# Optimization experiments

Measured on AMD Instinct MI355X. Metric: run time of the kernel, lower is better.

Reference implementation:

```python
import jax, jax.numpy as jnp
import numpy as np

N = 200000
E = 600000
C = 256


def setup_inputs() -> dict:
    key = jax.random.key(0)
    k1, k2, k3, k4, k5 = jax.random.split(key, 5)
    x = jax.random.normal(k1, (N, C), dtype=jnp.float32)
    sources = jax.random.randint(k2, (E,), 0, N, dtype=jnp.int64)
    targets = jax.random.randint(k3, (E,), 0, N, dtype=jnp.int64)
    norm = jax.random.uniform(k4, (N, 1), dtype=jnp.float32)
    # xavier_normal for [C, C]: std = sqrt(2 / (fan_in + fan_out))
    std = float(np.sqrt(2.0 / (C + C)))
    weight = jax.random.normal(k5, (C, C), dtype=jnp.float32) * std
    return {"x": x, "sources": sources, "targets": targets, "norm": norm, "weight": weight}


def reference(x, sources, targets, norm, weight):
    # out-of-place index_add: x + scatter_add(x[sources] -> targets)
    agg = x.at[targets].add(x[sources])  # [N, C]
    h = norm * agg                        # [N, C], norm broadcasts over channels
    return h @ weight                     # [N, C]
```

## Files before the change

kernel.cpp:

```cpp
#include <hip/hip_runtime.h>
#include <hip/hip_bf16.h>

#define NN 200000
#define NE 600000
#define CH 256
#define NBLK_SCAN 196

typedef short bf16x8 __attribute__((ext_vector_type(8)));
typedef float f32x4 __attribute__((ext_vector_type(4)));
typedef unsigned short ushort8v __attribute__((ext_vector_type(8)));

__device__ __forceinline__ unsigned short f2bf(float f) {
    unsigned int u = __builtin_bit_cast(unsigned int, f);
    u = (u + 0x7FFFu + ((u >> 16) & 1u)) >> 16;
    return (unsigned short)u;
}
__device__ __forceinline__ float bf2f(unsigned short u) {
    unsigned int v = ((unsigned int)u) << 16;
    return __builtin_bit_cast(float, v);
}

__global__ void k_wt(const float* __restrict__ W, unsigned short* __restrict__ Wt) {
    int j = blockIdx.x, k = threadIdx.x;
    Wt[j * CH + k] = f2bf(W[k * CH + j]);
}

__global__ __launch_bounds__(256) void k_prep(const float* __restrict__ W,
                                              unsigned short* __restrict__ Wt,
                                              const int* __restrict__ te,
                                              int* __restrict__ deg) {
    const int t = blockIdx.x * 256 + threadIdx.x;
    const int S = gridDim.x * 256;
    for (int e = t; e < NE; e += S) atomicAdd(&deg[te[e]], 1);
    for (int i = t; i < CH * CH; i += S) {
        int j = i >> 8, k = i & 255;
        Wt[j * CH + k] = f2bf(W[k * CH + j]);
    }
}

__global__ __launch_bounds__(256) void k_scanA(const int* __restrict__ deg,
                                               int* __restrict__ off,
                                               int* __restrict__ bsum) {
    __shared__ int ts[256];
    int tid = threadIdx.x;
    int base = blockIdx.x * 1024 + tid * 4;
    int v[4];
#pragma unroll
    for (int j = 0; j < 4; ++j) {
        int idx = base + j;
        v[j] = (idx < NN) ? deg[idx] : 0;
    }
    int tsum = v[0] + v[1] + v[2] + v[3];
    ts[tid] = tsum;
    __syncthreads();
    int x = tsum;
    for (int ofs = 1; ofs < 256; ofs <<= 1) {
        int y = (tid >= ofs) ? ts[tid - ofs] : 0;
        __syncthreads();
        x += y;
        ts[tid] = x;
        __syncthreads();
    }
    int run = x - tsum;
#pragma unroll
    for (int j = 0; j < 4; ++j) {
        int idx = base + j;
        if (idx < NN) off[idx] = run;
        run += v[j];
    }
    if (tid == 255) bsum[blockIdx.x] = x;
}

__global__ __launch_bounds__(256) void k_scanC(int* __restrict__ off,
                                               const int* __restrict__ bsum,
                                               int* __restrict__ cur) {
    __shared__ int ts[256];
    int tid = threadIdx.x;
    int v = (tid < NBLK_SCAN) ? bsum[tid] : 0;
    ts[tid] = v;
    __syncthreads();
    int x = v;
    for (int ofs = 1; ofs < 256; ofs <<= 1) {
        int y = (tid >= ofs) ? ts[tid - ofs] : 0;
        __syncthreads();
        x += y;
        ts[tid] = x;
        __syncthreads();
    }
    const int bo = (blockIdx.x == 0) ? 0 : ts[blockIdx.x - 1];
    int base = blockIdx.x * 1024 + tid * 4;
#pragma unroll
    for (int j = 0; j < 4; ++j) {
        int idx = base + j;
        if (idx < NN) {
            int o = off[idx] + bo;
            off[idx] = o;
            cur[idx] = o;
        }
    }
}

__global__ void k_fill(const int* __restrict__ se, const int* __restrict__ te,
                       int* __restrict__ cur, int* __restrict__ elist) {
    int e = blockIdx.x * 256 + threadIdx.x;
    if (e < NE) {
        int t = te[e];
        int pos = atomicAdd(&cur[t], 1);
        elist[pos] = se[e];
    }
}

__global__ __launch_bounds__(512, 4) void k_zw(const float* __restrict__ x,
                                               const unsigned short* __restrict__ Wt,
                                               unsigned short* __restrict__ zbf,
                                               const int* __restrict__ te,
                                               int* __restrict__ deg) {
    __shared__ unsigned short lds_a[128 * CH];
    const int tid = threadIdx.x;
    const int wid = tid >> 6;
    const int lane = tid & 63;
    const int wr = wid >> 2;
    const int wc = wid & 3;
    const int rb = blockIdx.x * 128;
    const int r16 = lane & 15;
    const int q = lane >> 4;
    const int vr = min(128, NN - rb);

    {
        const long long e = (long long)blockIdx.x * 512 + tid;
        if (e < NE) atomicAdd(&deg[te[e]], 1);
    }

#pragma unroll
    for (int i = 0; i < 8; ++i) {
        const int idx = i * 4096 + tid * 8;
        const int row = idx >> 8;
        const int col = idx & 255;
        const int srow = min(rb + row, NN - 1);
        const float* src = x + (size_t)srow * CH + col;
        float4 f0 = *reinterpret_cast<const float4*>(src);
        float4 f1 = *reinterpret_cast<const float4*>(src + 4);
        ushort8v w;
        w[0] = f2bf(f0.x); w[1] = f2bf(f0.y); w[2] = f2bf(f0.z); w[3] = f2bf(f0.w);
        w[4] = f2bf(f1.x); w[5] = f2bf(f1.y); w[6] = f2bf(f1.z); w[7] = f2bf(f1.w);
        const int gs = (col >> 3) ^ (row & 7);
        *reinterpret_cast<ushort8v*>(&lds_a[row * CH + gs * 8]) = w;
    }
    __syncthreads();

    f32x4 acc[4][4];
#pragma unroll
    for (int m = 0; m < 4; ++m)
#pragma unroll
        for (int nt = 0; nt < 4; ++nt) acc[m][nt] = (f32x4){0.f, 0.f, 0.f, 0.f};

    const unsigned short* wb = Wt + (size_t)(wc * 64 + r16) * CH + q * 8;

#pragma unroll
    for (int kk = 0; kk < 8; ++kk) {
        bf16x8 b[4];
#pragma unroll
        for (int nt = 0; nt < 4; ++nt)
            b[nt] = *reinterpret_cast<const bf16x8*>(wb + (size_t)nt * 16 * CH + kk * 32);
        bf16x8 a[4];
#pragma unroll
        for (int m = 0; m < 4; ++m) {
            const int lr = wr * 64 + m * 16 + r16;
            const int aidx = lr * CH + ((((kk * 4) + q) ^ (lr & 7)) << 3);
            a[m] = *reinterpret_cast<const bf16x8*>(&lds_a[aidx]);
        }
#pragma unroll
        for (int m = 0; m < 4; ++m)
#pragma unroll
            for (int nt = 0; nt < 4; ++nt)
                acc[m][nt] = __builtin_amdgcn_mfma_f32_16x16x32_bf16(a[m], b[nt], acc[m][nt], 0, 0, 0);
    }

    __syncthreads();
#pragma unroll
    for (int m = 0; m < 4; ++m) {
#pragma unroll
        for (int nt = 0; nt < 4; ++nt) {
            const int zr = wr * 64 + m * 16 + q * 4;
            const int zc = wc * 64 + nt * 16 + r16;
#pragma unroll
            for (int r = 0; r < 4; ++r)
                lds_a[(zr + r) * CH + zc] = f2bf(acc[m][nt][r]);
        }
    }
    __syncthreads();
    unsigned short* zdst = zbf + (size_t)rb * CH;
#pragma unroll
    for (int j = 0; j < 8; ++j) {
        const int idx = j * 4096 + tid * 8;
        const int row = idx >> 8;
        if (row < vr)
            *reinterpret_cast<ushort8v*>(zdst + idx) =
                *reinterpret_cast<const ushort8v*>(&lds_a[idx]);
    }
}

__global__ __launch_bounds__(256) void k_gout(const unsigned short* __restrict__ zbf,
                                              const int* __restrict__ off,
                                              const int* __restrict__ deg,
                                              const int* __restrict__ elist,
                                              const float* __restrict__ norm,
                                              float* __restrict__ out) {
    int wid = threadIdx.x >> 6;
    int lane = threadIdx.x & 63;
    int row = blockIdx.x * 4 + wid;
    if (row >= NN) return;
    int start = off[row];
    int d = deg[row];
    const int uo = lane * 4;
    ushort4 bv = *reinterpret_cast<const ushort4*>(zbf + (size_t)row * CH + uo);
    float ax = bf2f(bv.x), ay = bf2f(bv.y), az = bf2f(bv.z), aw = bf2f(bv.w);
    int e = 0;
    while (e < d) {
        int i0 = (e + 0 < d) ? elist[start + e + 0] : -1;
        int i1 = (e + 1 < d) ? elist[start + e + 1] : -1;
        int i2 = (e + 2 < d) ? elist[start + e + 2] : -1;
        int i3 = (e + 3 < d) ? elist[start + e + 3] : -1;
        int i4 = (e + 4 < d) ? elist[start + e + 4] : -1;
        int i5 = (e + 5 < d) ? elist[start + e + 5] : -1;
        int i6 = (e + 6 < d) ? elist[start + e + 6] : -1;
        int i7 = (e + 7 < d) ? elist[start + e + 7] : -1;
#define GACC(ii) if (ii >= 0) { \
            ushort4 v = *reinterpret_cast<const ushort4*>(zbf + (size_t)ii * CH + uo); \
            ax += bf2f(v.x); ay += bf2f(v.y); az += bf2f(v.z); aw += bf2f(v.w); }
        GACC(i0) GACC(i1) GACC(i2) GACC(i3) GACC(i4) GACC(i5) GACC(i6) GACC(i7)
#undef GACC
        e += 8;
    }
    const float nv = norm[row];
    float4 o;
    o.x = ax * nv; o.y = ay * nv; o.z = az * nv; o.w = aw * nv;
    *reinterpret_cast<float4*>(out + (size_t)row * CH + uo) = o;
}

__global__ __launch_bounds__(256, 4) void k_fgg(const float* __restrict__ x,
                                                const int* __restrict__ off,
                                                const int* __restrict__ deg,
                                                const int* __restrict__ elist,
                                                const float* __restrict__ norm,
                                                const unsigned short* __restrict__ Wt,
                                                float* __restrict__ out) {
    __shared__ unsigned short lds_a[64 * CH];
    const int tid = threadIdx.x;
    const int wid = tid >> 6;
    const int lane = tid & 63;
    const int rb = blockIdx.x * 64;
    const int rowbase = rb + wid * 16;
    const int r16 = lane & 15;
    const int q = lane >> 4;
    const int fo4 = lane * 4;

    const int offv = off[rowbase + r16];
    const int degv = deg[rowbase + r16];
    const float nv = norm[rb + lane];

    float4 acc[16];
#pragma unroll
    for (int r = 0; r < 16; ++r)
        acc[r] = *reinterpret_cast<const float4*>(x + (size_t)(rowbase + r) * CH + fo4);

#pragma unroll
    for (int r = 0; r < 16; ++r) {
        const int start = __shfl(offv, r);
        const int d = __shfl(degv, r);
        int e = 0;
        while (e < d) {
            int i0 = (e + 0 < d) ? elist[start + e + 0] : -1;
            int i1 = (e + 1 < d) ? elist[start + e + 1] : -1;
            int i2 = (e + 2 < d) ? elist[start + e + 2] : -1;
            int i3 = (e + 3 < d) ? elist[start + e + 3] : -1;
#define GACC(ii) if (ii >= 0) { \
            float4 v = *reinterpret_cast<const float4*>(x + (size_t)ii * CH + fo4); \
            acc[r].x += v.x; acc[r].y += v.y; acc[r].z += v.z; acc[r].w += v.w; }
            GACC(i0) GACC(i1) GACC(i2) GACC(i3)
#undef GACC
            e += 4;
        }
    }

    unsigned short* lb = lds_a + wid * 16 * CH;
#pragma unroll
    for (int r = 0; r < 16; ++r) {
        ushort4 w;
        w.x = f2bf(acc[r].x); w.y = f2bf(acc[r].y);
        w.z = f2bf(acc[r].z); w.w = f2bf(acc[r].w);
        const int gs = (lane >> 1) ^ (r & 7);
        *reinterpret_cast<ushort4*>(lb + r * CH + gs * 8 + (lane & 1) * 4) = w;
    }
    __syncthreads();

    f32x4 facc[4][4];
#pragma unroll
    for (int m = 0; m < 4; ++m)
#pragma unroll
        for (int nt = 0; nt < 4; ++nt) facc[m][nt] = (f32x4){0.f, 0.f, 0.f, 0.f};

    const unsigned short* wb = Wt + (size_t)(wid * 64 + r16) * CH + q * 8;

#pragma unroll
    for (int kk = 0; kk < 8; ++kk) {
        bf16x8 b[4];
#pragma unroll
        for (int nt = 0; nt < 4; ++nt)
            b[nt] = *reinterpret_cast<const bf16x8*>(wb + (size_t)nt * 16 * CH + kk * 32);
        bf16x8 a[4];
#pragma unroll
        for (int m = 0; m < 4; ++m) {
            const int lr = m * 16 + r16;
            const int idx = lr * CH + ((((kk * 4) + q) ^ (lr & 7)) << 3);
            a[m] = *reinterpret_cast<const bf16x8*>(&lds_a[idx]);
        }
#pragma unroll
        for (int m = 0; m < 4; ++m)
#pragma unroll
            for (int nt = 0; nt < 4; ++nt)
                facc[m][nt] = __builtin_amdgcn_mfma_f32_16x16x32_bf16(a[m], b[nt], facc[m][nt], 0, 0, 0);
    }

#pragma unroll
    for (int m = 0; m < 4; ++m) {
        const int crow = rb + m * 16 + q * 4;
#pragma unroll
        for (int nt = 0; nt < 4; ++nt) {
            float* po = out + (size_t)crow * CH + wid * 64 + nt * 16 + r16;
#pragma unroll
            for (int r = 0; r < 4; ++r) {
                const float nj = __shfl(nv, m * 16 + q * 4 + r);
                po[(size_t)r * CH] = facc[m][nt][r] * nj;
            }
        }
    }
}

extern "C" void kernel_launch(void* const* d_in, const int* in_sizes, int n_in,
                              void* d_out, int out_size, void* d_ws, size_t ws_size,
                              hipStream_t stream) {
    const float* x = (const float*)d_in[0];
    const int* se = (const int*)d_in[1];
    const int* te = (const int*)d_in[2];
    const float* norm = (const float*)d_in[3];
    const float* W = (const float*)d_in[4];
    float* out = (float*)d_out;

    char* ws = (char*)d_ws;
    unsigned short* Wt = (unsigned short*)ws;
    int* deg   = (int*)(ws + 131072);
    int* off   = (int*)(ws + 931072);
    int* cur   = (int*)(ws + 1731072);
    int* elist = (int*)(ws + 2531072);
    int* bsum  = (int*)(ws + 4931072);
    const size_t ZBF_OFF = 4932096;
    const size_t NEED = ZBF_OFF + (size_t)NN * CH * 2;
    const bool big = (ws_size >= NEED);
    unsigned short* zbf = (unsigned short*)(ws + ZBF_OFF);

    hipMemsetAsync(deg, 0, NN * sizeof(int), stream);
    if (big) {
        k_wt<<<CH, CH, 0, stream>>>(W, Wt);
        k_zw<<<(NN + 127) / 128, 512, 0, stream>>>(x, Wt, zbf, te, deg);
        k_scanA<<<NBLK_SCAN, 256, 0, stream>>>(deg, off, bsum);
        k_scanC<<<NBLK_SCAN, 256, 0, stream>>>(off, bsum, cur);
        k_fill<<<(NE + 255) / 256, 256, 0, stream>>>(se, te, cur, elist);
        k_gout<<<NN / 4, 256, 0, stream>>>(zbf, off, deg, elist, norm, out);
    } else {
        k_prep<<<512, 256, 0, stream>>>(W, Wt, te, deg);
        k_scanA<<<NBLK_SCAN, 256, 0, stream>>>(deg, off, bsum);
        k_scanC<<<NBLK_SCAN, 256, 0, stream>>>(off, bsum, cur);
        k_fill<<<(NE + 255) / 256, 256, 0, stream>>>(se, te, cur, elist);
        k_fgg<<<NN / 64, 256, 0, stream>>>(x, off, deg, elist, norm, Wt, out);
    }
}
```

Measured before the change: 263.2 us.

## Shrink k_zw tile to 32 rows and store MFMA results directly

The fused bf16 convert-and-matmul kernel now processes 32 rows per 256-thread block instead of 128 rows per 512-thread block. Its LDS footprint drops from 64 KB to 16 KB, which should allow more resident blocks, and all x loads are issued before the bf16 conversion. The epilogue drops the LDS round-trip and its two barriers: accumulators are written to global memory as scattered 2-byte stores. In exchange, each block rereads the full bf16 weight matrix from cache, roughly four times the total weight traffic, and the output stores are less coalesced.

Result: slower. 293.0 us (+11.3%).

```diff
diff --git a/kernel.cpp b/kernel.cpp
--- a/kernel.cpp
+++ b/kernel.cpp
@@ -5,6 +5,7 @@
 #define NE 600000
 #define CH 256
 #define NBLK_SCAN 196
+#define ZW_TILES 6250
 
 typedef short bf16x8 __attribute__((ext_vector_type(8)));
 typedef float f32x4 __attribute__((ext_vector_type(4)));
@@ -110,51 +111,54 @@
     }
 }
 
-__global__ __launch_bounds__(512, 4) void k_zw(const float* __restrict__ x,
+__global__ __launch_bounds__(256, 4) void k_zw(const float* __restrict__ x,
                                                const unsigned short* __restrict__ Wt,
                                                unsigned short* __restrict__ zbf,
                                                const int* __restrict__ te,
                                                int* __restrict__ deg) {
-    __shared__ unsigned short lds_a[128 * CH];
+    __shared__ unsigned short lds_a[32 * CH];
     const int tid = threadIdx.x;
     const int wid = tid >> 6;
     const int lane = tid & 63;
-    const int wr = wid >> 2;
-    const int wc = wid & 3;
-    const int rb = blockIdx.x * 128;
     const int r16 = lane & 15;
     const int q = lane >> 4;
-    const int vr = min(128, NN - rb);
+    const int rb = blockIdx.x * 32;
 
     {
-        const long long e = (long long)blockIdx.x * 512 + tid;
+        const int e = blockIdx.x * 256 + tid;
         if (e < NE) atomicAdd(&deg[te[e]], 1);
     }
 
-#pragma unroll
-    for (int i = 0; i < 8; ++i) {
-        const int idx = i * 4096 + tid * 8;
+    const float* gx = x + (size_t)rb * CH;
+    float4 st0[4], st1[4];
+#pragma unroll
+    for (int i = 0; i < 4; ++i) {
+        const int idx = i * 2048 + tid * 8;
+        st0[i] = *reinterpret_cast<const float4*>(gx + idx);
+        st1[i] = *reinterpret_cast<const float4*>(gx + idx + 4);
+    }
+#pragma unroll
+    for (int i = 0; i < 4; ++i) {
+        const int idx = i * 2048 + tid * 8;
         const int row = idx >> 8;
         const int col = idx & 255;
-        const int srow = min(rb + row, NN - 1);
-        const float* src = x + (size_t)srow * CH + col;
-        float4 f0 = *reinterpret_cast<const float4*>(src);
-        float4 f1 = *reinterpret_cast<const float4*>(src + 4);
         ushort8v w;
-        w[0] = f2bf(f0.x); w[1] = f2bf(f0.y); w[2] = f2bf(f0.z); w[3] = f2bf(f0.w);
-        w[4] = f2bf(f1.x); w[5] = f2bf(f1.y); w[6] = f2bf(f1.z); w[7] = f2bf(f1.w);
+        w[0] = f2bf(st0[i].x); w[1] = f2bf(st0[i].y);
+        w[2] = f2bf(st0[i].z); w[3] = f2bf(st0[i].w);
+        w[4] = f2bf(st1[i].x); w[5] = f2bf(st1[i].y);
+        w[6] = f2bf(st1[i].z); w[7] = f2bf(st1[i].w);
         const int gs = (col >> 3) ^ (row & 7);
         *reinterpret_cast<ushort8v*>(&lds_a[row * CH + gs * 8]) = w;
     }
     __syncthreads();
 
-    f32x4 acc[4][4];
-#pragma unroll
-    for (int m = 0; m < 4; ++m)
+    f32x4 acc[2][4];
+#pragma unroll
+    for (int m = 0; m < 2; ++m)
 #pragma unroll
         for (int nt = 0; nt < 4; ++nt) acc[m][nt] = (f32x4){0.f, 0.f, 0.f, 0.f};
 
-    const unsigned short* wb = Wt + (size_t)(wc * 64 + r16) * CH + q * 8;
+    const unsigned short* wb = Wt + (size_t)(wid * 64 + r16) * CH + q * 8;
 
 #pragma unroll
     for (int kk = 0; kk < 8; ++kk) {
@@ -162,41 +166,29 @@
 #pragma unroll
         for (int nt = 0; nt < 4; ++nt)
             b[nt] = *reinterpret_cast<const bf16x8*>(wb + (size_t)nt * 16 * CH + kk * 32);
-        bf16x8 a[4];
-#pragma unroll
-        for (int m = 0; m < 4; ++m) {
-            const int lr = wr * 64 + m * 16 + r16;
+        bf16x8 a[2];
+#pragma unroll
+        for (int m = 0; m < 2; ++m) {
+            const int lr = m * 16 + r16;
             const int aidx = lr * CH + ((((kk * 4) + q) ^ (lr & 7)) << 3);
             a[m] = *reinterpret_cast<const bf16x8*>(&lds_a[aidx]);
         }
 #pragma unroll
-        for (int m = 0; m < 4; ++m)
+        for (int m = 0; m < 2; ++m)
 #pragma unroll
             for (int nt = 0; nt < 4; ++nt)
                 acc[m][nt] = __builtin_amdgcn_mfma_f32_16x16x32_bf16(a[m], b[nt], acc[m][nt], 0, 0, 0);
     }
 
-    __syncthreads();
-#pragma unroll
-    for (int m = 0; m < 4; ++m) {
+#pragma unroll
+    for (int m = 0; m < 2; ++m) {
 #pragma unroll
         for (int nt = 0; nt < 4; ++nt) {
-            const int zr = wr * 64 + m * 16 + q * 4;
-            const int zc = wc * 64 + nt * 16 + r16;
-#pragma unroll
-            for (int r = 0; r < 4; ++r)
-                lds_a[(zr + r) * CH + zc] = f2bf(acc[m][nt][r]);
-        }
-    }
-    __syncthreads();
-    unsigned short* zdst = zbf + (size_t)rb * CH;
-#pragma unroll
-    for (int j = 0; j < 8; ++j) {
-        const int idx = j * 4096 + tid * 8;
-        const int row = idx >> 8;
-        if (row < vr)
-            *reinterpret_cast<ushort8v*>(zdst + idx) =
-                *reinterpret_cast<const ushort8v*>(&lds_a[idx]);
+            unsigned short* po = zbf + (size_t)(rb + m * 16 + q * 4) * CH
+                               + wid * 64 + nt * 16 + r16;
+#pragma unroll
+            for (int r = 0; r < 4; ++r) po[(size_t)r * CH] = f2bf(acc[m][nt][r]);
+        }
     }
 }
 
@@ -362,7 +354,7 @@
     hipMemsetAsync(deg, 0, NN * sizeof(int), stream);
     if (big) {
         k_wt<<<CH, CH, 0, stream>>>(W, Wt);
-        k_zw<<<(NN + 127) / 128, 512, 0, stream>>>(x, Wt, zbf, te, deg);
+        k_zw<<<ZW_TILES, 256, 0, stream>>>(x, Wt, zbf, te, deg);
         k_scanA<<<NBLK_SCAN, 256, 0, stream>>>(deg, off, bsum);
         k_scanC<<<NBLK_SCAN, 256, 0, stream>>>(off, bsum, cur);
         k_fill<<<(NE + 255) / 256, 256, 0, stream>>>(se, te, cur, elist);
```
